# Kernel optimization log

Hardware: AMD Instinct MI355X
Metric: run time of the kernel (lower is better)

Reference implementation:

```python
import jax, jax.numpy as jnp
import numpy as np

# Grid parameters (from init_kwargs)
GRID_W, GRID_L, GRID_H = 96, 96, 48
VOXEL_SIZE = 0.05
MIN_POINTS_PER_VOXEL = 10


def setup_inputs() -> dict:
    key = jax.random.key(0)
    k1, k2 = jax.random.split(key, 2)
    # points uniform over a ~[0,1.5]^3 sub-volume so voxel occupancy is realistic
    point_coordinates = jax.random.uniform(k1, (4, 3, 480, 640), jnp.float32) * 1.5
    point_attributes = jax.random.normal(k2, (4, 16, 480, 640), jnp.float32)
    origin = jnp.zeros((4, 3), jnp.float32)
    return {"point_coordinates": point_coordinates,
            "point_attributes": point_attributes,
            "origin": origin}


def _voxelize_one(coords, attrs, org):
    # coords: [3, N], attrs: [C, N], org: [3]
    V = GRID_W * GRID_L * GRID_H
    bounds = jnp.array([GRID_W, GRID_L, GRID_H], jnp.int32)
    # per-point voxel index (floor == .long() for positive; OOB handled by mask)
    idx3 = jnp.floor((coords - org[:, None]) / VOXEL_SIZE).astype(jnp.int32)  # [3, N]
    in_bounds = jnp.all((idx3 >= 0) & (idx3 < bounds[:, None]), axis=0)       # [N]
    flat = idx3[0] * (GRID_L * GRID_H) + idx3[1] * GRID_H + idx3[2]           # [N]
    flat = jnp.where(in_bounds, flat, 0)  # route OOB points to voxel 0, masked out
    # occupancy: scatter-add of in-bounds mask
    counts = jax.ops.segment_sum(in_bounds.astype(jnp.float32), flat, num_segments=V)
    # max-pool of attributes per voxel; OOB points contribute -inf
    masked = jnp.where(in_bounds[None, :], attrs, -jnp.inf)                   # [C, N]
    vmax = jax.ops.segment_max(masked.T, flat, num_segments=V).T              # [C, V]
    occ = counts >= MIN_POINTS_PER_VOXEL                                      # [V]
    data = jnp.where(occ[None, :] & jnp.isfinite(vmax), vmax, 0.0)            # [C, V]
    return data, occ


def reference(point_coordinates, point_attributes, origin):
    b, c = point_attributes.shape[:2]
    coords = point_coordinates.reshape(b, 3, -1)   # [B, 3, N]
    attrs = point_attributes.reshape(b, c, -1)     # [B, C, N]
    data, occ = jax.vmap(_voxelize_one)(coords, attrs, origin)
    voxeldata = data.reshape(b, c, GRID_W, GRID_L, GRID_H)
    voxeloccupancy = occ.reshape(b, 1, GRID_W, GRID_L, GRID_H).astype(jnp.float32)
    return voxeldata, voxeloccupancy
```

## Files before the change

kernel.cpp:

```cpp
#include <hip/hip_runtime.h>
#include <cstdint>
#include <math.h>

#define GRID_W 96
#define GRID_L 96
#define GRID_H 48
#define NVOX (GRID_W * GRID_L * GRID_H)
#define VOXEL_SIZE 0.05f
#define MIN_PTS 10
#define BATCH 4
#define CHANS 16
#define NPTS (480 * 640)
#define TOTPTS (BATCH * NPTS)
#define TOTVOX (BATCH * NVOX)

#define SCAN_BLKS 864
#define SCAN_TPB 256
#define SCAN_EPT 8
#define SCAN_CHUNK (SCAN_TPB * SCAN_EPT)

#define ROWW 8

#define WS_OFFSETS 0
#define WS_VR      ((TOTVOX + 4) * 4)
#define WS_ROWS    (WS_VR + TOTPTS * 4)
#define WS_SUMS    (WS_ROWS + (size_t)TOTPTS * ROWW * 4)
#define WS_NEEDED  ((size_t)(WS_SUMS + 4096))

__device__ __forceinline__ unsigned bf16_rtne(float f) {
    unsigned u = __float_as_uint(f);
    return (u + 0x7FFFu + ((u >> 16) & 1u)) >> 16;
}
__device__ __forceinline__ unsigned pack2(float lo, float hi) {
    return bf16_rtne(lo) | (bf16_rtne(hi) << 16);
}


__global__ void k_hist4(const float* __restrict__ coords,
                        const float* __restrict__ origin,
                        unsigned*    __restrict__ vr,
                        unsigned*    __restrict__ cnt)
{
    int t = blockIdx.x * blockDim.x + threadIdx.x;
    if (t >= TOTPTS / 4) return;
    int pid = t * 4;
    int b = pid / NPTS;
    int n = pid - b * NPTS;

    const float* cb = coords + (size_t)b * 3 * NPTS;
    float4 X = *(const float4*)(cb + n);
    float4 Y = *(const float4*)(cb + NPTS + n);
    float4 Z = *(const float4*)(cb + 2 * NPTS + n);
    float ox = origin[b * 3 + 0];
    float oy = origin[b * 3 + 1];
    float oz = origin[b * 3 + 2];

    float xs[4] = {X.x, X.y, X.z, X.w};
    float ys[4] = {Y.x, Y.y, Y.z, Y.w};
    float zs[4] = {Z.x, Z.y, Z.z, Z.w};
    unsigned ps[4];
    #pragma unroll
    for (int k = 0; k < 4; ++k) {
        int ix = (int)floorf((xs[k] - ox) / VOXEL_SIZE);
        int iy = (int)floorf((ys[k] - oy) / VOXEL_SIZE);
        int iz = (int)floorf((zs[k] - oz) / VOXEL_SIZE);
        unsigned p = 0xFFFFFFFFu;
        if ((unsigned)ix < GRID_W && (unsigned)iy < GRID_L && (unsigned)iz < GRID_H) {
            int v = b * NVOX + ix * (GRID_L * GRID_H) + iy * GRID_H + iz;
            unsigned r = atomicAdd(&cnt[v], 1u);
            p = ((unsigned)v << 10) | (r & 1023u);
        }
        ps[k] = p;
    }
    *(uint4*)(vr + pid) = uint4{ps[0], ps[1], ps[2], ps[3]};
}

__global__ void k_scan1(unsigned* __restrict__ offsets,
                        unsigned* __restrict__ sums,
                        float*    __restrict__ occ)
{
    __shared__ unsigned s[SCAN_TPB];
    int t = threadIdx.x;
    int base = blockIdx.x * SCAN_CHUNK + t * SCAN_EPT;

    uint4 a = ((const uint4*)(offsets + base))[0];
    uint4 c = ((const uint4*)(offsets + base))[1];
    unsigned e[SCAN_EPT] = {a.x, a.y, a.z, a.w, c.x, c.y, c.z, c.w};

    float4 oc0, oc1;
    oc0.x = (e[0] >= MIN_PTS) ? 1.f : 0.f;  oc0.y = (e[1] >= MIN_PTS) ? 1.f : 0.f;
    oc0.z = (e[2] >= MIN_PTS) ? 1.f : 0.f;  oc0.w = (e[3] >= MIN_PTS) ? 1.f : 0.f;
    oc1.x = (e[4] >= MIN_PTS) ? 1.f : 0.f;  oc1.y = (e[5] >= MIN_PTS) ? 1.f : 0.f;
    oc1.z = (e[6] >= MIN_PTS) ? 1.f : 0.f;  oc1.w = (e[7] >= MIN_PTS) ? 1.f : 0.f;
    ((float4*)(occ + base))[0] = oc0;
    ((float4*)(occ + base))[1] = oc1;

    unsigned tot = 0;
    #pragma unroll
    for (int k = 0; k < SCAN_EPT; ++k) { unsigned v = e[k]; e[k] = tot; tot += v; }

    s[t] = tot;
    __syncthreads();
    #pragma unroll
    for (int off = 1; off < SCAN_TPB; off <<= 1) {
        unsigned v = (t >= off) ? s[t - off] : 0u;
        __syncthreads();
        s[t] += v;
        __syncthreads();
    }
    unsigned prefix = s[t] - tot;
    #pragma unroll
    for (int k = 0; k < SCAN_EPT; ++k) e[k] += prefix;

    ((uint4*)(offsets + base))[0] = uint4{e[0], e[1], e[2], e[3]};
    ((uint4*)(offsets + base))[1] = uint4{e[4], e[5], e[6], e[7]};

    if (t == SCAN_TPB - 1) sums[blockIdx.x] = s[t];
}

__global__ void k_scan2(unsigned* __restrict__ sums) {
    __shared__ unsigned s[1024];
    int t = threadIdx.x;
    unsigned my = (t < SCAN_BLKS) ? sums[t] : 0u;
    s[t] = my;
    __syncthreads();
    #pragma unroll
    for (int off = 1; off < 1024; off <<= 1) {
        unsigned v = (t >= off) ? s[t - off] : 0u;
        __syncthreads();
        s[t] += v;
        __syncthreads();
    }
    if (t < SCAN_BLKS) sums[t] = s[t] - my;
    if (t == SCAN_BLKS - 1) sums[SCAN_BLKS] = s[t];
}

__global__ void k_scatter_rows4(const float*    __restrict__ attrs,
                                const unsigned* __restrict__ vr,
                                const unsigned* __restrict__ offsets,
                                const unsigned* __restrict__ sums,
                                unsigned*       __restrict__ rows)
{
    int t = blockIdx.x * blockDim.x + threadIdx.x;
    if (t >= TOTPTS / 4) return;
    int pid = t * 4;
    int b = pid / NPTS;
    int n = pid - b * NPTS;

    uint4 P = *(const uint4*)(vr + pid);
    unsigned ps[4] = {P.x, P.y, P.z, P.w};
    unsigned pos[4];
    #pragma unroll
    for (int k = 0; k < 4; ++k) {
        pos[k] = 0xFFFFFFFFu;
        if (ps[k] != 0xFFFFFFFFu) {
            unsigned v = ps[k] >> 10;
            pos[k] = offsets[v] + sums[v >> 11] + (ps[k] & 1023u);
        }
    }

    const float* ab = attrs + (size_t)b * CHANS * NPTS + n;
    unsigned w[4][ROWW];
    #pragma unroll
    for (int c = 0; c < CHANS; c += 2) {
        float4 a0 = *(const float4*)(ab + (size_t)c * NPTS);
        float4 a1 = *(const float4*)(ab + (size_t)(c + 1) * NPTS);
        w[0][c >> 1] = pack2(a0.x, a1.x);
        w[1][c >> 1] = pack2(a0.y, a1.y);
        w[2][c >> 1] = pack2(a0.z, a1.z);
        w[3][c >> 1] = pack2(a0.w, a1.w);
    }
    #pragma unroll
    for (int k = 0; k < 4; ++k) {
        if (pos[k] == 0xFFFFFFFFu) continue;
        uint4* dst = (uint4*)(rows + (size_t)pos[k] * ROWW);
        dst[0] = uint4{w[k][0], w[k][1], w[k][2], w[k][3]};
        dst[1] = uint4{w[k][4], w[k][5], w[k][6], w[k][7]};
    }
}

__global__ void k_gather_rows4(const unsigned* __restrict__ rows,
                               const unsigned* __restrict__ offsets,
                               const unsigned* __restrict__ sums,
                               float*          __restrict__ data)
{
    int g = blockIdx.x * blockDim.x + threadIdx.x;
    if (g >= TOTVOX / 4) return;
    int vox0 = g * 4;

    uint4 O = *(const uint4*)(offsets + vox0);
    unsigned base = sums[vox0 >> 11];
    unsigned s[5];
    s[0] = O.x + base; s[1] = O.y + base; s[2] = O.z + base; s[3] = O.w + base;
    s[4] = offsets[vox0 + 4] + sums[(vox0 + 4) >> 11];

    float m[4][CHANS];
    #pragma unroll
    for (int q = 0; q < 4; ++q) {
        unsigned k = s[q + 1] - s[q];
        if (k >= MIN_PTS) {
            const float ninf = -__builtin_inff();
            #pragma unroll
            for (int c = 0; c < CHANS; ++c) m[q][c] = ninf;
            const uint4* seg = (const uint4*)(rows + (size_t)s[q] * ROWW);
            for (unsigned j = 0; j < k; ++j) {
                uint4 lo = seg[0], hi = seg[1];
                seg += 2;
                unsigned ww[8] = {lo.x, lo.y, lo.z, lo.w, hi.x, hi.y, hi.z, hi.w};
                #pragma unroll
                for (int h = 0; h < 8; ++h) {
                    float f0 = __uint_as_float(ww[h] << 16);
                    float f1 = __uint_as_float(ww[h] & 0xFFFF0000u);
                    m[q][2 * h]     = fmaxf(m[q][2 * h], f0);
                    m[q][2 * h + 1] = fmaxf(m[q][2 * h + 1], f1);
                }
            }
            #pragma unroll
            for (int c = 0; c < CHANS; ++c) if (!isfinite(m[q][c])) m[q][c] = 0.f;
        } else {
            #pragma unroll
            for (int c = 0; c < CHANS; ++c) m[q][c] = 0.f;
        }
    }

    int b = vox0 / NVOX;
    int v0 = vox0 - b * NVOX;
    float* db = data + (size_t)b * CHANS * NVOX + v0;
    #pragma unroll
    for (int c = 0; c < CHANS; ++c) {
        *(float4*)(db + (size_t)c * NVOX) = float4{m[0][c], m[1][c], m[2][c], m[3][c]};
    }
}


__device__ __forceinline__ unsigned flip_f32(float f) {
    unsigned u = __float_as_uint(f);
    unsigned mask = (unsigned)(-(int)(u >> 31)) | 0x80000000u;
    return u ^ mask;
}
__device__ __forceinline__ float unflip_f32(unsigned u) {
    unsigned mask = ((u >> 31) - 1u) | 0x80000000u;
    return __uint_as_float(u ^ mask);
}
#define FLIP_NEG_INF 0x007FFFFFu

__global__ void pv_init(uint4* __restrict__ out) {
    const int DATA4 = BATCH * CHANS * NVOX / 4;
    const int TOT4  = BATCH * (CHANS + 1) * NVOX / 4;
    int i = blockIdx.x * blockDim.x + threadIdx.x;
    if (i < TOT4) {
        unsigned val = (i < DATA4) ? FLIP_NEG_INF : 0u;
        out[i] = uint4{val, val, val, val};
    }
}

__global__ void pv_scatter(const float* __restrict__ coords,
                           const float* __restrict__ attrs,
                           const float* __restrict__ origin,
                           unsigned*    __restrict__ data_u,
                           unsigned*    __restrict__ cnt)
{
    int id = blockIdx.x * blockDim.x + threadIdx.x;
    if (id >= TOTPTS) return;
    int b = id / NPTS;
    int n = id - b * NPTS;
    const float* cb = coords + (size_t)b * 3 * NPTS;
    float x = cb[n], y = cb[NPTS + n], z = cb[2 * NPTS + n];
    float ox = origin[b * 3 + 0], oy = origin[b * 3 + 1], oz = origin[b * 3 + 2];
    int ix = (int)floorf((x - ox) / VOXEL_SIZE);
    int iy = (int)floorf((y - oy) / VOXEL_SIZE);
    int iz = (int)floorf((z - oz) / VOXEL_SIZE);
    if ((unsigned)ix < GRID_W && (unsigned)iy < GRID_L && (unsigned)iz < GRID_H) {
        int flat = ix * (GRID_L * GRID_H) + iy * GRID_H + iz;
        atomicAdd(&cnt[b * NVOX + flat], 1u);
        const float* ab = attrs + (size_t)b * CHANS * NPTS + n;
        unsigned*    db = data_u + (size_t)b * CHANS * NVOX + flat;
        #pragma unroll
        for (int c = 0; c < CHANS; ++c)
            atomicMax(&db[(size_t)c * NVOX], flip_f32(ab[(size_t)c * NPTS]));
    }
}

__global__ void pv_finalize(unsigned* __restrict__ data_u,
                            unsigned* __restrict__ cnt_u)
{
    int id = blockIdx.x * blockDim.x + threadIdx.x;
    if (id >= TOTVOX) return;
    int b = id / NVOX;
    int v = id - b * NVOX;
    unsigned cnt = cnt_u[id];
    bool occ = (cnt >= MIN_PTS);
    ((float*)cnt_u)[id] = occ ? 1.0f : 0.0f;
    unsigned* db = data_u + (size_t)b * CHANS * NVOX + v;
    #pragma unroll
    for (int c = 0; c < CHANS; ++c) {
        float f = unflip_f32(db[(size_t)c * NVOX]);
        ((float*)db)[(size_t)c * NVOX] = (occ && isfinite(f)) ? f : 0.0f;
    }
}


extern "C" void kernel_launch(void* const* d_in, const int* in_sizes, int n_in,
                              void* d_out, int out_size, void* d_ws, size_t ws_size,
                              hipStream_t stream) {
    const float* coords = (const float*)d_in[0];
    const float* attrs  = (const float*)d_in[1];
    const float* origin = (const float*)d_in[2];

    float* out = (float*)d_out;
    float* data = out;
    float* occ  = out + (size_t)BATCH * CHANS * NVOX;

    if (ws_size >= WS_NEEDED) {
        char* ws = (char*)d_ws;
        unsigned* offsets = (unsigned*)(ws + WS_OFFSETS);
        unsigned* vr      = (unsigned*)(ws + WS_VR);
        unsigned* rows    = (unsigned*)(ws + WS_ROWS);
        unsigned* sums    = (unsigned*)(ws + WS_SUMS);

        hipMemsetAsync(offsets, 0, (size_t)(TOTVOX + 4) * 4, stream);
        k_hist4<<<(TOTPTS / 4 + 255) / 256, 256, 0, stream>>>(coords, origin, vr, offsets);
        k_scan1<<<SCAN_BLKS, SCAN_TPB, 0, stream>>>(offsets, sums, occ);
        k_scan2<<<1, 1024, 0, stream>>>(sums);
        k_scatter_rows4<<<(TOTPTS / 4 + 255) / 256, 256, 0, stream>>>(attrs, vr, offsets, sums, rows);
        k_gather_rows4<<<(TOTVOX / 4 + 255) / 256, 256, 0, stream>>>(rows, offsets, sums, data);
    } else {
        unsigned* data_u = (unsigned*)data;
        unsigned* cnt    = (unsigned*)occ;
        const int TOT4 = BATCH * (CHANS + 1) * NVOX / 4;
        pv_init<<<(TOT4 + 255) / 256, 256, 0, stream>>>((uint4*)d_out);
        pv_scatter<<<(TOTPTS + 255) / 256, 256, 0, stream>>>(coords, attrs, origin, data_u, cnt);
        pv_finalize<<<(TOTVOX + 255) / 256, 256, 0, stream>>>(data_u, cnt);
    }
}
```

Baseline: 337.3 us.

## Pack bf16 rows in point order during histogram and gather via index list

```diff
diff --git a/kernel.cpp b/kernel.cpp
--- a/kernel.cpp
+++ b/kernel.cpp
@@ -23,7 +23,8 @@
 
 #define WS_OFFSETS 0
 #define WS_VR      ((TOTVOX + 4) * 4)
-#define WS_ROWS    (WS_VR + TOTPTS * 4)
+#define WS_IDS     (WS_VR + TOTPTS * 4)
+#define WS_ROWS    (WS_IDS + TOTPTS * 4 + 16)
 #define WS_SUMS    (WS_ROWS + (size_t)TOTPTS * ROWW * 4)
 #define WS_NEEDED  ((size_t)(WS_SUMS + 4096))
 
@@ -36,10 +37,12 @@
 }
 
 
-__global__ void k_hist4(const float* __restrict__ coords,
-                        const float* __restrict__ origin,
-                        unsigned*    __restrict__ vr,
-                        unsigned*    __restrict__ cnt)
+__global__ void k_hist_pack(const float* __restrict__ coords,
+                            const float* __restrict__ attrs,
+                            const float* __restrict__ origin,
+                            unsigned*    __restrict__ vr,
+                            unsigned*    __restrict__ rows,
+                            unsigned*    __restrict__ cnt)
 {
     int t = blockIdx.x * blockDim.x + threadIdx.x;
     if (t >= TOTPTS / 4) return;
@@ -54,6 +57,24 @@
     float ox = origin[b * 3 + 0];
     float oy = origin[b * 3 + 1];
     float oz = origin[b * 3 + 2];
+
+    const float* ab = attrs + (size_t)b * CHANS * NPTS + n;
+    unsigned w[4][ROWW];
+    #pragma unroll
+    for (int c = 0; c < CHANS; c += 2) {
+        float4 a0 = *(const float4*)(ab + (size_t)c * NPTS);
+        float4 a1 = *(const float4*)(ab + (size_t)(c + 1) * NPTS);
+        w[0][c >> 1] = pack2(a0.x, a1.x);
+        w[1][c >> 1] = pack2(a0.y, a1.y);
+        w[2][c >> 1] = pack2(a0.z, a1.z);
+        w[3][c >> 1] = pack2(a0.w, a1.w);
+    }
+    #pragma unroll
+    for (int k = 0; k < 4; ++k) {
+        uint4* dst = (uint4*)(rows + (size_t)(pid + k) * ROWW);
+        dst[0] = uint4{w[k][0], w[k][1], w[k][2], w[k][3]};
+        dst[1] = uint4{w[k][4], w[k][5], w[k][6], w[k][7]};
+    }
 
     float xs[4] = {X.x, X.y, X.z, X.w};
     float ys[4] = {Y.x, Y.y, Y.z, Y.w};
@@ -135,54 +156,31 @@
     if (t == SCAN_BLKS - 1) sums[SCAN_BLKS] = s[t];
 }
 
-__global__ void k_scatter_rows4(const float*    __restrict__ attrs,
-                                const unsigned* __restrict__ vr,
-                                const unsigned* __restrict__ offsets,
-                                const unsigned* __restrict__ sums,
-                                unsigned*       __restrict__ rows)
+__global__ void k_scatter_ids4(const unsigned* __restrict__ vr,
+                               const unsigned* __restrict__ offsets,
+                               const unsigned* __restrict__ sums,
+                               int*            __restrict__ ids)
 {
     int t = blockIdx.x * blockDim.x + threadIdx.x;
     if (t >= TOTPTS / 4) return;
     int pid = t * 4;
-    int b = pid / NPTS;
-    int n = pid - b * NPTS;
-
     uint4 P = *(const uint4*)(vr + pid);
     unsigned ps[4] = {P.x, P.y, P.z, P.w};
-    unsigned pos[4];
     #pragma unroll
     for (int k = 0; k < 4; ++k) {
-        pos[k] = 0xFFFFFFFFu;
         if (ps[k] != 0xFFFFFFFFu) {
             unsigned v = ps[k] >> 10;
-            pos[k] = offsets[v] + sums[v >> 11] + (ps[k] & 1023u);
+            unsigned pos = offsets[v] + sums[v >> 11] + (ps[k] & 1023u);
+            ids[pos] = pid + k;
         }
     }
-
-    const float* ab = attrs + (size_t)b * CHANS * NPTS + n;
-    unsigned w[4][ROWW];
-    #pragma unroll
-    for (int c = 0; c < CHANS; c += 2) {
-        float4 a0 = *(const float4*)(ab + (size_t)c * NPTS);
-        float4 a1 = *(const float4*)(ab + (size_t)(c + 1) * NPTS);
-        w[0][c >> 1] = pack2(a0.x, a1.x);
-        w[1][c >> 1] = pack2(a0.y, a1.y);
-        w[2][c >> 1] = pack2(a0.z, a1.z);
-        w[3][c >> 1] = pack2(a0.w, a1.w);
-    }
-    #pragma unroll
-    for (int k = 0; k < 4; ++k) {
-        if (pos[k] == 0xFFFFFFFFu) continue;
-        uint4* dst = (uint4*)(rows + (size_t)pos[k] * ROWW);
-        dst[0] = uint4{w[k][0], w[k][1], w[k][2], w[k][3]};
-        dst[1] = uint4{w[k][4], w[k][5], w[k][6], w[k][7]};
-    }
-}
-
-__global__ void k_gather_rows4(const unsigned* __restrict__ rows,
-                               const unsigned* __restrict__ offsets,
-                               const unsigned* __restrict__ sums,
-                               float*          __restrict__ data)
+}
+
+__global__ void k_gather_ind4(const unsigned* __restrict__ rows,
+                              const int*      __restrict__ ids,
+                              const unsigned* __restrict__ offsets,
+                              const unsigned* __restrict__ sums,
+                              float*          __restrict__ data)
 {
     int g = blockIdx.x * blockDim.x + threadIdx.x;
     if (g >= TOTVOX / 4) return;
@@ -198,21 +196,41 @@
     #pragma unroll
     for (int q = 0; q < 4; ++q) {
         unsigned k = s[q + 1] - s[q];
+        unsigned s0 = s[q];
         if (k >= MIN_PTS) {
             const float ninf = -__builtin_inff();
             #pragma unroll
             for (int c = 0; c < CHANS; ++c) m[q][c] = ninf;
-            const uint4* seg = (const uint4*)(rows + (size_t)s[q] * ROWW);
-            for (unsigned j = 0; j < k; ++j) {
-                uint4 lo = seg[0], hi = seg[1];
-                seg += 2;
-                unsigned ww[8] = {lo.x, lo.y, lo.z, lo.w, hi.x, hi.y, hi.z, hi.w};
+            unsigned j = 0;
+            for (; j + 2 <= k; j += 2) {
+                int p0 = ids[s0 + j];
+                int p1 = ids[s0 + j + 1];
+                const uint4* r0p = (const uint4*)(rows + (size_t)p0 * ROWW);
+                const uint4* r1p = (const uint4*)(rows + (size_t)p1 * ROWW);
+                uint4 l0 = r0p[0], h0 = r0p[1];
+                uint4 l1 = r1p[0], h1 = r1p[1];
+                unsigned wa[8] = {l0.x, l0.y, l0.z, l0.w, h0.x, h0.y, h0.z, h0.w};
+                unsigned wb[8] = {l1.x, l1.y, l1.z, l1.w, h1.x, h1.y, h1.z, h1.w};
                 #pragma unroll
                 for (int h = 0; h < 8; ++h) {
-                    float f0 = __uint_as_float(ww[h] << 16);
-                    float f1 = __uint_as_float(ww[h] & 0xFFFF0000u);
-                    m[q][2 * h]     = fmaxf(m[q][2 * h], f0);
-                    m[q][2 * h + 1] = fmaxf(m[q][2 * h + 1], f1);
+                    m[q][2 * h]     = fmaxf(m[q][2 * h],
+                                        fmaxf(__uint_as_float(wa[h] << 16),
+                                              __uint_as_float(wb[h] << 16)));
+                    m[q][2 * h + 1] = fmaxf(m[q][2 * h + 1],
+                                        fmaxf(__uint_as_float(wa[h] & 0xFFFF0000u),
+                                              __uint_as_float(wb[h] & 0xFFFF0000u)));
+                }
+            }
+            if (j < k) {
+                int p0 = ids[s0 + j];
+                const uint4* r0p = (const uint4*)(rows + (size_t)p0 * ROWW);
+                uint4 l0 = r0p[0], h0 = r0p[1];
+                unsigned wa[8] = {l0.x, l0.y, l0.z, l0.w, h0.x, h0.y, h0.z, h0.w};
+                #pragma unroll
+                for (int h = 0; h < 8; ++h) {
+                    m[q][2 * h]     = fmaxf(m[q][2 * h], __uint_as_float(wa[h] << 16));
+                    m[q][2 * h + 1] = fmaxf(m[q][2 * h + 1],
+                                            __uint_as_float(wa[h] & 0xFFFF0000u));
                 }
             }
             #pragma unroll
@@ -315,15 +333,17 @@
         char* ws = (char*)d_ws;
         unsigned* offsets = (unsigned*)(ws + WS_OFFSETS);
         unsigned* vr      = (unsigned*)(ws + WS_VR);
+        int*      ids     = (int*)(ws + WS_IDS);
         unsigned* rows    = (unsigned*)(ws + WS_ROWS);
         unsigned* sums    = (unsigned*)(ws + WS_SUMS);
 
         hipMemsetAsync(offsets, 0, (size_t)(TOTVOX + 4) * 4, stream);
-        k_hist4<<<(TOTPTS / 4 + 255) / 256, 256, 0, stream>>>(coords, origin, vr, offsets);
+        k_hist_pack<<<(TOTPTS / 4 + 255) / 256, 256, 0, stream>>>(coords, attrs, origin,
+                                                                  vr, rows, offsets);
         k_scan1<<<SCAN_BLKS, SCAN_TPB, 0, stream>>>(offsets, sums, occ);
         k_scan2<<<1, 1024, 0, stream>>>(sums);
-        k_scatter_rows4<<<(TOTPTS / 4 + 255) / 256, 256, 0, stream>>>(attrs, vr, offsets, sums, rows);
-        k_gather_rows4<<<(TOTVOX / 4 + 255) / 256, 256, 0, stream>>>(rows, offsets, sums, data);
+        k_scatter_ids4<<<(TOTPTS / 4 + 255) / 256, 256, 0, stream>>>(vr, offsets, sums, ids);
+        k_gather_ind4<<<(TOTVOX / 4 + 255) / 256, 256, 0, stream>>>(rows, ids, offsets, sums, data);
     } else {
         unsigned* data_u = (unsigned*)data;
         unsigned* cnt    = (unsigned*)occ;
```

New measurement: 313.4 us. 1.08x faster.
